# Kernel optimization log

Measured on AMD Instinct MI355X. Metric: run time of the kernel, lower is better.

Reference implementation:

```python
import jax, jax.numpy as jnp
import numpy as np
import math

DIM = 768
HEADS = 12
HEAD_DIM = DIM // HEADS
SCALE_PARAM_INIT = 1.0 / math.sqrt(DIM)  # Scale(scale=1/sqrt(dim), init=1.0)


def cosine_norm(x, eps=1e-6):
    norm = jnp.maximum(jnp.linalg.norm(x, axis=-1, keepdims=True), eps)
    return x / norm


def setup_inputs() -> dict:
    key = jax.random.key(0)
    ks = jax.random.split(key, 6)
    B, N = 8, 1024
    x = jax.random.normal(ks[0], (B, N, DIM), dtype=jnp.float32)
    # torch nn.Linear weights are [out, in]; y = x @ W^T
    std = 1.0 / math.sqrt(DIM)
    Wq = jax.random.uniform(ks[1], (DIM, DIM), jnp.float32, -std, std)
    Wk = jax.random.uniform(ks[2], (DIM, DIM), jnp.float32, -std, std)
    Wv = jax.random.uniform(ks[3], (DIM, DIM), jnp.float32, -std, std)
    Wo = jax.random.uniform(ks[4], (DIM, DIM), jnp.float32, -std, std)
    # Scale param s: ones * scale, perturbed slightly for generality
    s_qk = SCALE_PARAM_INIT * (1.0 + 0.1 * jax.random.normal(ks[5], (HEADS, HEAD_DIM), jnp.float32))
    return {"x": x, "Wq": Wq, "Wk": Wk, "Wv": Wv, "Wo": Wo, "s_qk": s_qk}


def reference(x, Wq, Wk, Wv, Wo, s_qk):
    B, N, _ = x.shape
    # projections (torch Linear: x @ W^T)
    q = (x @ Wq.T).reshape(B, N, HEADS, HEAD_DIM)
    k = (x @ Wk.T).reshape(B, N, HEADS, HEAD_DIM)
    v = (x @ Wv.T).reshape(B, N, HEADS, HEAD_DIM)
    # effective scale = s * (init / scale)
    s_eff = s_qk * (1.0 / SCALE_PARAM_INIT)  # [H, D]
    q = cosine_norm(q) * s_eff  # broadcast over [B, N, H, D]
    k = cosine_norm(k) * s_eff
    scale = HEAD_DIM ** 0.5  # note: multiplies logits (nGPT-style)
    # [B, H, N, N]
    logits = jnp.einsum('bqhd,bkhd->bhqk', q, k) * scale
    attn = jax.nn.softmax(logits, axis=-1)
    out = jnp.einsum('bhqk,bkhd->bqhd', attn, v).reshape(B, N, HEADS * HEAD_DIM)
    return out @ Wo.T
```

## Files before the change

kernel.cpp:

```cpp
#include <hip/hip_runtime.h>
#include <hip/hip_bf16.h>
#include <math.h>

#define NDIM 768
#define NHEADS 12
#define HD 64
#define SEQ 1024
#define BATCH 8
#define MROWS (BATCH * SEQ)
#define SQRT_DIM 27.712812921102035f
#define LOG2E 1.4426950408889634f

typedef unsigned short u16;
typedef unsigned int u32;
typedef __attribute__((ext_vector_type(8))) short short8;
typedef __attribute__((ext_vector_type(4))) short bf16x4;
typedef __attribute__((ext_vector_type(4))) float f32x4;
typedef __attribute__((ext_vector_type(16))) float f32x16;

#define MFMA16(a, b, c) __builtin_amdgcn_mfma_f32_16x16x32_bf16(a, b, c, 0, 0, 0)
#define MFMA32(a, b, c) __builtin_amdgcn_mfma_f32_32x32x16_bf16(a, b, c, 0, 0, 0)

#if __has_builtin(__builtin_amdgcn_exp2f)
#define EXP2(x) __builtin_amdgcn_exp2f(x)
#else
#define EXP2(x) exp2f(x)
#endif

__device__ inline u16 f2bf(float f) {
    __hip_bfloat16 h = __float2bfloat16(f);
    return *reinterpret_cast<u16*>(&h);
}

__device__ inline u32 rne_pack(float a, float b) {
    u32 ua = __builtin_bit_cast(u32, a), ub = __builtin_bit_cast(u32, b);
    ua = (ua + 0x7fffu + ((ua >> 16) & 1u)) >> 16;
    ub = (ub + 0x7fffu + ((ub >> 16) & 1u)) >> 16;
    return (ub << 16) | ua;
}

__device__ inline void gl2lds16(const void* g, void* l) {
    __builtin_amdgcn_global_load_lds((const __attribute__((address_space(1))) void*)g,
                                     (__attribute__((address_space(3))) void*)l, 16, 0, 0);
}

__global__ __launch_bounds__(256) void castall(const float* __restrict__ x,
                                               const float* __restrict__ Wq,
                                               const float* __restrict__ Wk,
                                               const float* __restrict__ Wv,
                                               const float* __restrict__ Wo,
                                               u16* __restrict__ xb,
                                               u16* __restrict__ Wqkv,
                                               u16* __restrict__ Wob) {
    const int WB = (NDIM * NDIM) / 1024;
    int blk = blockIdx.x;
    const float* s;
    u16* d;
    int base;
    if (blk < 6144) {
        s = x; d = xb; base = blk * 1024;
    } else {
        int wsel = (blk - 6144) / WB, r = (blk - 6144) % WB;
        base = r * 1024;
        if (wsel == 0)      { s = Wq; d = Wqkv; }
        else if (wsel == 1) { s = Wk; d = Wqkv + NDIM * NDIM; }
        else if (wsel == 2) { s = Wv; d = Wqkv + 2 * NDIM * NDIM; }
        else                { s = Wo; d = Wob; }
    }
    int i = base + threadIdx.x * 4;
    float4 v = *(const float4*)(s + i);
    uint2 o = make_uint2(rne_pack(v.x, v.y), rne_pack(v.z, v.w));
    *(uint2*)(d + i) = o;
}

template <int EPI>
__global__ __launch_bounds__(256) void gemm_bf16(const u16* __restrict__ A,
                                                 const u16* __restrict__ B,
                                                 void* __restrict__ C, int N,
                                                 const float* __restrict__ s_qk,
                                                 u16* __restrict__ Qdst,
                                                 u16* __restrict__ Kdst,
                                                 int NX) {
    constexpr int K = NDIM;
    constexpr int NKT = K / 32;
    __shared__ __align__(16) u16 As[2][4096];
    __shared__ __align__(16) u16 Bs[2][4096];
    const int t = threadIdx.x;
    const int wave = t >> 6, lane = t & 63;
    const int quad = lane >> 4, l16 = lane & 15;
    const int wx = (wave & 1) * 64, wy = (wave >> 1) * 64;
    const int blk = blockIdx.x;
    const int xcd = blk & 7, local = blk >> 3;
    const int bm = (xcd * 8 + local / NX) * 128;
    const int bn = (local % NX) * 128;

    f32x4 acc[4][4];
#pragma unroll
    for (int i = 0; i < 4; ++i)
#pragma unroll
        for (int j = 0; j < 4; ++j) acc[i][j] = (f32x4){0.f, 0.f, 0.f, 0.f};

    const int srl = lane >> 2;
    const int skc = (lane & 3) ^ ((lane >> 3) & 3);
    auto stage = [&](int k0, int bsel) {
#pragma unroll
        for (int it = 0; it < 2; ++it) {
            const int cb = it * 256 + wave * 64;
            const int row = (cb >> 6) * 16 + srl;
            gl2lds16(A + (size_t)(bm + row) * K + k0 + skc * 8,
                     (char*)As[bsel] + cb * 16);
            gl2lds16(B + (size_t)(bn + row) * K + k0 + skc * 8,
                     (char*)Bs[bsel] + cb * 16);
        }
    };
    const int fxor = (l16 >> 1) & 3;

    stage(0, 0);
#pragma unroll
    for (int kt = 0; kt < NKT; ++kt) {
        __syncthreads();
        if (kt + 1 < NKT) stage((kt + 1) * 32, (kt + 1) & 1);
        const int b = kt & 1;
        short8 af[4], bfr[4];
#pragma unroll
        for (int i = 0; i < 4; ++i)
            af[i] = *(const short8*)&As[b][
                ((((wy >> 4) + i) * 64 + l16 * 4 + (quad ^ fxor)) * 8)];
#pragma unroll
        for (int j = 0; j < 4; ++j)
            bfr[j] = *(const short8*)&Bs[b][
                ((((wx >> 4) + j) * 64 + l16 * 4 + (quad ^ fxor)) * 8)];
#pragma unroll
        for (int i = 0; i < 4; ++i)
#pragma unroll
            for (int j = 0; j < 4; ++j) acc[i][j] = MFMA16(af[i], bfr[j], acc[i][j]);
    }

    if constexpr (EPI == 0) {
#pragma unroll
        for (int i = 0; i < 4; ++i)
#pragma unroll
            for (int j = 0; j < 4; ++j)
#pragma unroll
                for (int r = 0; r < 4; ++r) {
                    const int row = bm + wy + i * 16 + quad * 4 + r;
                    const int col = bn + wx + j * 16 + l16;
                    ((float*)C)[(size_t)row * N + col] = acc[i][j][r];
                }
    } else {
        const int cg = (bn + wx) >> 6;
        if (cg >= 2 * NHEADS) {
            const int h = cg - 2 * NHEADS;
#pragma unroll
            for (int i = 0; i < 4; ++i)
#pragma unroll
                for (int j = 0; j < 4; ++j)
#pragma unroll
                    for (int r = 0; r < 4; ++r) {
                        const int row = bm + wy + i * 16 + quad * 4 + r;
                        const int dd = j * 16 + l16;
                        const int b = row >> 10, n = row & 1023;
                        ((u16*)C)[(((size_t)(b * NHEADS + h) * HD + dd) << 10) + n] =
                            f2bf(acc[i][j][r]);
                    }
        } else {
            const bool isq = cg < NHEADS;
            const int h = isq ? cg : cg - NHEADS;
            u16* dst = isq ? Qdst : Kdst;
            const float ex = isq ? 8.f * LOG2E : 1.f;
            float sq[4];
#pragma unroll
            for (int j = 0; j < 4; ++j)
                sq[j] = s_qk[h * HD + j * 16 + l16] * SQRT_DIM * ex;
#pragma unroll
            for (int i = 0; i < 4; ++i)
#pragma unroll
                for (int r = 0; r < 4; ++r) {
                    float ss = 0.f;
#pragma unroll
                    for (int j = 0; j < 4; ++j) ss += acc[i][j][r] * acc[i][j][r];
                    ss += __shfl_xor(ss, 1, 64);
                    ss += __shfl_xor(ss, 2, 64);
                    ss += __shfl_xor(ss, 4, 64);
                    ss += __shfl_xor(ss, 8, 64);
                    float inv = 1.f / fmaxf(sqrtf(ss), 1e-6f);
                    const int row = bm + wy + i * 16 + quad * 4 + r;
                    const int b = row >> 10, tok = row & 1023;
                    u16* o = dst + ((size_t)(b * NHEADS + h) * SEQ + tok) * HD;
#pragma unroll
                    for (int j = 0; j < 4; ++j)
                        o[j * 16 + l16] = f2bf(acc[i][j][r] * sq[j] * inv);
                }
        }
    }
}

__global__ __launch_bounds__(256) void attn_mfma(const u16* __restrict__ Qh,
                                                 const u16* __restrict__ Kh,
                                                 const u16* __restrict__ Vt,
                                                 u16* __restrict__ AO) {
    __shared__ __align__(16) u16 Ks[512 * 8];
    __shared__ __align__(16) u16 Vs[512 * 8];
    __shared__ __align__(16) u16 Ps[4 * 32 * 64];

    const int t = threadIdx.x;
    const int wave = t >> 6, lane = t & 63;
    const int l31 = lane & 31, half = lane >> 5;
    const int b = blockIdx.z, h = blockIdx.y, q0 = blockIdx.x * 128;
    const int bh = b * NHEADS + h;
    const u16* Kb = Kh + (size_t)bh * SEQ * HD;
    const u16* Vb = Vt + (size_t)bh * HD * SEQ;
    const int qb = q0 + wave * 32;
    const int pbase = wave * 2048 + l31 * 64;
    const int sw = (l31 & 15);

    short8 qf[4];
#pragma unroll
    for (int tt = 0; tt < 4; ++tt)
        qf[tt] = *(const short8*)(Qh + ((size_t)bh * SEQ + qb + l31) * HD +
                                  tt * 16 + half * 8);

    f32x16 o[2];
#pragma unroll
    for (int dt = 0; dt < 2; ++dt)
#pragma unroll
        for (int r = 0; r < 16; ++r) o[dt][r] = 0.f;
    float lp = 0.f;

    const int arl = lane >> 3;
    const int acc8 = (lane & 7) ^ arl;
    const int fx8 = l31 & 7;

    for (int j0 = 0; j0 < SEQ; j0 += 64) {
        __syncthreads();
#pragma unroll
        for (int it = 0; it < 2; ++it) {
            const int cb = it * 256 + wave * 64;
            const int r0 = (cb >> 6) * 8 + arl;
            gl2lds16(Kb + (size_t)(j0 + r0) * HD + acc8 * 8, (char*)Ks + cb * 16);
            gl2lds16(Vb + (size_t)r0 * SEQ + j0 + acc8 * 8, (char*)Vs + cb * 16);
        }
        asm volatile("s_waitcnt vmcnt(0)" ::: "memory");
        __syncthreads();

#pragma unroll
        for (int kt = 0; kt < 2; ++kt) {
            f32x16 sa;
#pragma unroll
            for (int r = 0; r < 16; ++r) sa[r] = 0.f;
#pragma unroll
            for (int tt = 0; tt < 4; ++tt) {
                short8 kf = *(const short8*)&Ks[
                    (((kt * 4 + (l31 >> 3)) * 64) + fx8 * 8 +
                     ((2 * tt + half) ^ fx8)) * 8];
                sa = MFMA32(kf, qf[tt], sa);
            }
#pragma unroll
            for (int rg = 0; rg < 4; ++rg) {
                float p0 = EXP2(sa[rg * 4 + 0]);
                float p1 = EXP2(sa[rg * 4 + 1]);
                float p2 = EXP2(sa[rg * 4 + 2]);
                float p3 = EXP2(sa[rg * 4 + 3]);
                lp += (p0 + p1) + (p2 + p3);
                uint2 pk = make_uint2(rne_pack(p0, p1), rne_pack(p2, p3));
                const int u = kt * 8 + rg * 2 + half;
                *(uint2*)&Ps[pbase + (u ^ sw) * 4] = pk;
            }
        }

#pragma unroll
        for (int k2 = 0; k2 < 4; ++k2) {
            const int u0 = k2 * 4 + half * 2;
            bf16x4 lo = *(const bf16x4*)&Ps[pbase + ((u0 + 0) ^ sw) * 4];
            bf16x4 hi = *(const bf16x4*)&Ps[pbase + ((u0 + 1) ^ sw) * 4];
            short8 pf = __builtin_shufflevector(lo, hi, 0, 1, 2, 3, 4, 5, 6, 7);
#pragma unroll
            for (int dt = 0; dt < 2; ++dt) {
                short8 vf = *(const short8*)&Vs[
                    (((dt * 4 + (l31 >> 3)) * 64) + fx8 * 8 +
                     ((2 * k2 + half) ^ fx8)) * 8];
                o[dt] = MFMA32(vf, pf, o[dt]);
            }
        }
    }

    const float invl = 1.f / (lp + __shfl_xor(lp, 32, 64));
    u16* ob = AO + (size_t)(b * SEQ + qb + l31) * NDIM + h * HD;
#pragma unroll
    for (int dt = 0; dt < 2; ++dt)
#pragma unroll
        for (int rg = 0; rg < 4; ++rg) {
            bf16x4 ok = {(short)f2bf(o[dt][rg * 4 + 0] * invl),
                         (short)f2bf(o[dt][rg * 4 + 1] * invl),
                         (short)f2bf(o[dt][rg * 4 + 2] * invl),
                         (short)f2bf(o[dt][rg * 4 + 3] * invl)};
            *(bf16x4*)(ob + dt * 32 + rg * 8 + half * 4) = ok;
        }
}

extern "C" void kernel_launch(void* const* d_in, const int* in_sizes, int n_in,
                              void* d_out, int out_size, void* d_ws, size_t ws_size,
                              hipStream_t stream) {
    const float* x    = (const float*)d_in[0];
    const float* Wq   = (const float*)d_in[1];
    const float* Wk   = (const float*)d_in[2];
    const float* Wv   = (const float*)d_in[3];
    const float* Wo   = (const float*)d_in[4];
    const float* s_qk = (const float*)d_in[5];
    float* out = (float*)d_out;

    char* w = (char*)d_ws;
    const size_t TE = (size_t)MROWS * NDIM;
    u16* xb   = (u16*)w;                    w += TE * 2;
    u16* Wqkv = (u16*)w;                    w += (size_t)3 * NDIM * NDIM * 2;
    u16* Wob  = (u16*)w;                    w += (size_t)NDIM * NDIM * 2;
    u16* Qh   = (u16*)w;                    w += TE * 2;
    u16* Kh   = (u16*)w;                    w += TE * 2;
    u16* Vt   = (u16*)w;                    w += TE * 2;
    u16* ao   = (u16*)w;

    castall<<<6144 + 4 * 576, 256, 0, stream>>>(x, Wq, Wk, Wv, Wo, xb, Wqkv, Wob);

    gemm_bf16<2><<<18 * 64, 256, 0, stream>>>(
        xb, Wqkv, (void*)Vt, 2304, s_qk, Qh, Kh, 18);

    attn_mfma<<<dim3(SEQ / 128, NHEADS, BATCH), 256, 0, stream>>>(Qh, Kh, Vt, ao);

    gemm_bf16<0><<<6 * 64, 256, 0, stream>>>(
        ao, Wob, out, NDIM, nullptr, nullptr, nullptr, 6);
}
```

Before: 198.8 us.

## Add 256x256-tile 8-wave QKV GEMM with ping-pong LDS staging

Replaces the 128x128-tile QKV projection GEMM with a dedicated 512-thread kernel that computes 256x256 output tiles using BK=64 and XOR-swizzled LDS buffers. It interleaves global-to-LDS staging of the next A/B sub-tiles with four MFMA phases per k-step, using explicit barriers, waitcnt and s_setprio to overlap loads with compute. The larger tiles raise arithmetic intensity and cut redundant global reads, and the grid is remapped across XCDs. The cost is higher register and LDS pressure, which may lower occupancy, and a 288-block grid that may fill the GPU's CUs unevenly. The fused normalization and scatter epilogue is carried over to the new tile shape.

```diff
diff --git a/kernel.cpp b/kernel.cpp
--- a/kernel.cpp
+++ b/kernel.cpp
@@ -43,6 +43,13 @@
     __builtin_amdgcn_global_load_lds((const __attribute__((address_space(1))) void*)g,
                                      (__attribute__((address_space(3))) void*)l, 16, 0, 0);
 }
+
+__device__ inline void bar() {
+    asm volatile("" ::: "memory");
+    __builtin_amdgcn_s_barrier();
+    asm volatile("" ::: "memory");
+}
+#define LGKM0 asm volatile("s_waitcnt lgkmcnt(0)" ::: "memory")
 
 __global__ __launch_bounds__(256) void castall(const float* __restrict__ x,
                                                const float* __restrict__ Wq,
@@ -73,6 +80,201 @@
     *(uint2*)(d + i) = o;
 }
 
+__global__ __launch_bounds__(512, 2) void gemm256_qkv(const u16* __restrict__ A,
+                                                      const u16* __restrict__ B,
+                                                      u16* __restrict__ Vt,
+                                                      const float* __restrict__ s_qk,
+                                                      u16* __restrict__ Qdst,
+                                                      u16* __restrict__ Kdst) {
+    constexpr int K = NDIM;
+    constexpr int NT = K / 64;
+    __shared__ __align__(16) u16 As[2][2][128 * 64];
+    __shared__ __align__(16) u16 Bs[2][2][128 * 64];
+
+    const int t = threadIdx.x;
+    const int wave = t >> 6, lane = t & 63;
+    const int quad = lane >> 4, l16 = lane & 15;
+    const int wm = wave >> 2, wn = wave & 3;
+    const int fx = l16 & 7;
+
+    const int wgid = (blockIdx.x & 7) * 36 + (blockIdx.x >> 3);
+    const int bm = (wgid / 9) * 256;
+    const int bn = (wgid % 9) * 256;
+
+    f32x4 acc[8][4];
+#pragma unroll
+    for (int i = 0; i < 8; ++i)
+#pragma unroll
+        for (int j = 0; j < 4; ++j) acc[i][j] = (f32x4){0.f, 0.f, 0.f, 0.f};
+
+    const int srow = lane >> 3;
+    const int schk = (lane & 7) ^ srow;
+    auto stg = [&](const u16* src, u16* dst) {
+#pragma unroll
+        for (int it = 0; it < 2; ++it) {
+            const int cb = it * 512 + wave * 64;
+            const int r = (cb >> 3) + srow;
+            gl2lds16(src + (size_t)r * K + schk * 8, (char*)dst + cb * 16);
+        }
+    };
+    const u16* Ag = A + (size_t)bm * K;
+    const u16* Bg = B + (size_t)bn * K;
+
+    stg(Ag,                        As[0][0]);
+    stg(Ag + (size_t)128 * K,      As[0][1]);
+    stg(Bg,                        Bs[0][0]);
+    stg(Bg + (size_t)128 * K,      Bs[0][1]);
+    stg(Bg + 64,                   Bs[1][0]);
+    stg(Bg + (size_t)128 * K + 64, Bs[1][1]);
+    asm volatile("s_waitcnt vmcnt(4)" ::: "memory");
+    bar();
+
+    short8 a[4][2], b0[2][2], b1[2][2];
+    const int rb0 = (wn & 1) * 64;
+
+#pragma unroll 2
+    for (int T = 0; T < NT; ++T) {
+        const int db = T & 1;
+        u16* Asl = As[db][wm];
+        u16* Bsl = Bs[db][wn >> 1];
+        const u16* An = Ag + (size_t)(T + 1) * 64;
+        const u16* Bn = Bg + (size_t)(T + 2) * 64;
+
+#pragma unroll
+        for (int mi = 0; mi < 4; ++mi) {
+            const int r = mi * 16 + l16;
+#pragma unroll
+            for (int kk = 0; kk < 2; ++kk)
+                a[mi][kk] = *(const short8*)&Asl[(r * 8 + ((kk * 4 + quad) ^ fx)) * 8];
+        }
+#pragma unroll
+        for (int ni = 0; ni < 2; ++ni) {
+            const int r = rb0 + ni * 16 + l16;
+#pragma unroll
+            for (int kk = 0; kk < 2; ++kk)
+                b0[ni][kk] = *(const short8*)&Bsl[(r * 8 + ((kk * 4 + quad) ^ fx)) * 8];
+        }
+        if (T + 1 < NT) stg(An, As[db ^ 1][0]);
+        bar();
+        LGKM0;
+        __builtin_amdgcn_s_setprio(1);
+#pragma unroll
+        for (int kk = 0; kk < 2; ++kk)
+#pragma unroll
+            for (int mi = 0; mi < 4; ++mi)
+#pragma unroll
+                for (int ni = 0; ni < 2; ++ni)
+                    acc[mi][ni] = MFMA16(a[mi][kk], b0[ni][kk], acc[mi][ni]);
+        __builtin_amdgcn_s_setprio(0);
+        bar();
+
+#pragma unroll
+        for (int ni = 0; ni < 2; ++ni) {
+            const int r = rb0 + (ni + 2) * 16 + l16;
+#pragma unroll
+            for (int kk = 0; kk < 2; ++kk)
+                b1[ni][kk] = *(const short8*)&Bsl[(r * 8 + ((kk * 4 + quad) ^ fx)) * 8];
+        }
+        if (T + 1 < NT) stg(An + (size_t)128 * K, As[db ^ 1][1]);
+        bar();
+        LGKM0;
+        __builtin_amdgcn_s_setprio(1);
+#pragma unroll
+        for (int kk = 0; kk < 2; ++kk)
+#pragma unroll
+            for (int mi = 0; mi < 4; ++mi)
+#pragma unroll
+                for (int ni = 0; ni < 2; ++ni)
+                    acc[mi][ni + 2] = MFMA16(a[mi][kk], b1[ni][kk], acc[mi][ni + 2]);
+        __builtin_amdgcn_s_setprio(0);
+        bar();
+
+#pragma unroll
+        for (int mi = 0; mi < 4; ++mi) {
+            const int r = (mi + 4) * 16 + l16;
+#pragma unroll
+            for (int kk = 0; kk < 2; ++kk)
+                a[mi][kk] = *(const short8*)&Asl[(r * 8 + ((kk * 4 + quad) ^ fx)) * 8];
+        }
+        if (T + 2 < NT) stg(Bn, Bs[db][0]);
+        bar();
+        LGKM0;
+        __builtin_amdgcn_s_setprio(1);
+#pragma unroll
+        for (int kk = 0; kk < 2; ++kk)
+#pragma unroll
+            for (int mi = 0; mi < 4; ++mi)
+#pragma unroll
+                for (int ni = 0; ni < 2; ++ni)
+                    acc[mi + 4][ni + 2] = MFMA16(a[mi][kk], b1[ni][kk], acc[mi + 4][ni + 2]);
+        __builtin_amdgcn_s_setprio(0);
+        bar();
+
+        if (T + 2 < NT) stg(Bn + (size_t)128 * K, Bs[db][1]);
+        bar();
+        __builtin_amdgcn_s_setprio(1);
+#pragma unroll
+        for (int kk = 0; kk < 2; ++kk)
+#pragma unroll
+            for (int mi = 0; mi < 4; ++mi)
+#pragma unroll
+                for (int ni = 0; ni < 2; ++ni)
+                    acc[mi + 4][ni] = MFMA16(a[mi][kk], b0[ni][kk], acc[mi + 4][ni]);
+        __builtin_amdgcn_s_setprio(0);
+        if (T + 2 < NT) {
+            asm volatile("s_waitcnt vmcnt(4)" ::: "memory");
+        } else {
+            asm volatile("s_waitcnt vmcnt(0)" ::: "memory");
+        }
+        bar();
+    }
+
+    const int cg = (bn + wn * 64) >> 6;
+    if (cg >= 2 * NHEADS) {
+        const int h = cg - 2 * NHEADS;
+#pragma unroll
+        for (int mi = 0; mi < 8; ++mi)
+#pragma unroll
+            for (int ni = 0; ni < 4; ++ni)
+#pragma unroll
+                for (int r = 0; r < 4; ++r) {
+                    const int row = bm + wm * 128 + mi * 16 + quad * 4 + r;
+                    const int dd = ni * 16 + l16;
+                    const int bb = row >> 10, n = row & 1023;
+                    Vt[(((size_t)(bb * NHEADS + h) * HD + dd) << 10) + n] =
+                        f2bf(acc[mi][ni][r]);
+                }
+    } else {
+        const bool isq = cg < NHEADS;
+        const int h = isq ? cg : cg - NHEADS;
+        u16* dst = isq ? Qdst : Kdst;
+        const float ex = isq ? 8.f * LOG2E : 1.f;
+        float sq[4];
+#pragma unroll
+        for (int ni = 0; ni < 4; ++ni)
+            sq[ni] = s_qk[h * HD + ni * 16 + l16] * SQRT_DIM * ex;
+#pragma unroll
+        for (int mi = 0; mi < 8; ++mi)
+#pragma unroll
+            for (int r = 0; r < 4; ++r) {
+                float ss = 0.f;
+#pragma unroll
+                for (int ni = 0; ni < 4; ++ni) ss += acc[mi][ni][r] * acc[mi][ni][r];
+                ss += __shfl_xor(ss, 1, 64);
+                ss += __shfl_xor(ss, 2, 64);
+                ss += __shfl_xor(ss, 4, 64);
+                ss += __shfl_xor(ss, 8, 64);
+                float inv = 1.f / fmaxf(sqrtf(ss), 1e-6f);
+                const int row = bm + wm * 128 + mi * 16 + quad * 4 + r;
+                const int bb = row >> 10, tok = row & 1023;
+                u16* o = dst + ((size_t)(bb * NHEADS + h) * SEQ + tok) * HD;
+#pragma unroll
+                for (int ni = 0; ni < 4; ++ni)
+                    o[ni * 16 + l16] = f2bf(acc[mi][ni][r] * sq[ni] * inv);
+            }
+    }
+}
+
 template <int EPI>
 __global__ __launch_bounds__(256) void gemm_bf16(const u16* __restrict__ A,
                                                  const u16* __restrict__ B,
@@ -147,51 +349,6 @@
                     const int col = bn + wx + j * 16 + l16;
                     ((float*)C)[(size_t)row * N + col] = acc[i][j][r];
                 }
-    } else {
-        const int cg = (bn + wx) >> 6;
-        if (cg >= 2 * NHEADS) {
-            const int h = cg - 2 * NHEADS;
-#pragma unroll
-            for (int i = 0; i < 4; ++i)
-#pragma unroll
-                for (int j = 0; j < 4; ++j)
-#pragma unroll
-                    for (int r = 0; r < 4; ++r) {
-                        const int row = bm + wy + i * 16 + quad * 4 + r;
-                        const int dd = j * 16 + l16;
-                        const int b = row >> 10, n = row & 1023;
-                        ((u16*)C)[(((size_t)(b * NHEADS + h) * HD + dd) << 10) + n] =
-                            f2bf(acc[i][j][r]);
-                    }
-        } else {
-            const bool isq = cg < NHEADS;
-            const int h = isq ? cg : cg - NHEADS;
-            u16* dst = isq ? Qdst : Kdst;
-            const float ex = isq ? 8.f * LOG2E : 1.f;
-            float sq[4];
-#pragma unroll
-            for (int j = 0; j < 4; ++j)
-                sq[j] = s_qk[h * HD + j * 16 + l16] * SQRT_DIM * ex;
-#pragma unroll
-            for (int i = 0; i < 4; ++i)
-#pragma unroll
-                for (int r = 0; r < 4; ++r) {
-                    float ss = 0.f;
-#pragma unroll
-                    for (int j = 0; j < 4; ++j) ss += acc[i][j][r] * acc[i][j][r];
-                    ss += __shfl_xor(ss, 1, 64);
-                    ss += __shfl_xor(ss, 2, 64);
-                    ss += __shfl_xor(ss, 4, 64);
-                    ss += __shfl_xor(ss, 8, 64);
-                    float inv = 1.f / fmaxf(sqrtf(ss), 1e-6f);
-                    const int row = bm + wy + i * 16 + quad * 4 + r;
-                    const int b = row >> 10, tok = row & 1023;
-                    u16* o = dst + ((size_t)(b * NHEADS + h) * SEQ + tok) * HD;
-#pragma unroll
-                    for (int j = 0; j < 4; ++j)
-                        o[j * 16 + l16] = f2bf(acc[i][j][r] * sq[j] * inv);
-                }
-        }
     }
 }
 
@@ -321,8 +478,7 @@
 
     castall<<<6144 + 4 * 576, 256, 0, stream>>>(x, Wq, Wk, Wv, Wo, xb, Wqkv, Wob);
 
-    gemm_bf16<2><<<18 * 64, 256, 0, stream>>>(
-        xb, Wqkv, (void*)Vt, 2304, s_qk, Qh, Kh, 18);
+    gemm256_qkv<<<288, 512, 0, stream>>>(xb, Wqkv, Vt, s_qk, Qh, Kh);
 
     attn_mfma<<<dim3(SEQ / 128, NHEADS, BATCH), 256, 0, stream>>>(Qh, Kh, Vt, ao);
 
```

Result: slower. 203.3 us (+2.2%).
